# Optimization experiments

Hardware: AMD Instinct MI355X
Metric: run time of the kernel (lower is better)

The kernel has to match this reference:

```python
import jax, jax.numpy as jnp
import numpy as np
from jax.scipy.special import logsumexp

N, K, D = 131072, 256, 32


def setup_inputs() -> dict:
    key = jax.random.key(0)
    k1, k2, k3 = jax.random.split(key, 3)
    points = jax.random.normal(k1, (N, D), dtype=jnp.float32)
    centers = jax.random.uniform(k2, (K, D), dtype=jnp.float32)
    # well-conditioned inverse-sqrt covariances (original used 15*I; scaled to
    # avoid float32 overflow in sqrt(det(covs_inv)) for D=32)
    covs_inv_sqrt = (0.5 * jnp.broadcast_to(jnp.eye(D, dtype=jnp.float32), (K, D, D))
                     + 0.02 * jax.random.normal(k3, (K, D, D), dtype=jnp.float32))
    weights = jnp.ones((K,), dtype=jnp.float32)
    threshold = jnp.zeros((1,), dtype=jnp.float32)
    return {"points": points, "centers": centers,
            "covs_inv_sqrt": covs_inv_sqrt, "weights": weights,
            "threshold": threshold}


def reference(points, centers, covs_inv_sqrt, weights, threshold):
    # refresh(): equal_clusters=True branch
    w = jnp.abs(weights)
    center_prs = w / (w.sum() + 1e-30)                       # [K]
    covs_inv = jnp.einsum('kde,kfe->kdf', covs_inv_sqrt, covs_inv_sqrt)  # [K,D,D]
    coefs = center_prs * jnp.sqrt(jnp.linalg.det(covs_inv))  # [K]

    # pairwise weighted sqdist: q_ij = (x_i - c_j)^T A_j (x_i - c_j)
    B = covs_inv.reshape(K, D * D)                           # [K, D*D]
    X2 = (points[:, :, None] * points[:, None, :]).reshape(N, D * D)  # [N, D*D]
    t_xAx = X2 @ B.T                                         # [N, K]
    m = jnp.einsum('kde,ke->kd', covs_inv, centers)          # A_j c_j, [K,D]
    t_xAc = points @ m.T                                     # [N, K]
    t_cAc = jnp.einsum('kd,kd->k', m, centers)               # [K]
    d_ij = -0.5 * (t_xAx - 2.0 * t_xAc + t_cAc[None, :])     # [N, K]

    # weighted logsumexp over centers, then subtract threshold
    ll = logsumexp(d_ij, axis=1, b=coefs[None, :])           # [N]
    return ll[:, None] - threshold[0]                        # [N, 1]
```

## Files before the change

### kernel.cpp

```cpp
#include <hip/hip_runtime.h>
#include <math.h>

#define NPTS 131072
#define KCOMP 256
#define DIM 32
#define KF 608
#define PSIF_BYTES 311296
#define WS_NEED (PSIF_BYTES + KCOMP * 4)

typedef __attribute__((ext_vector_type(8))) short short8;
typedef __attribute__((ext_vector_type(16))) float f32x16;

__device__ __forceinline__ unsigned short f2bf(float v) {
    unsigned u = __float_as_uint(v);
    u += 0x7fffu + ((u >> 16) & 1u);
    return (unsigned short)(u >> 16);
}

__device__ __forceinline__ unsigned pkbf(float lo, float hi) {
#if __has_builtin(__builtin_amdgcn_perm)
    const unsigned a = __float_as_uint(hi) + 0x8000u;
    const unsigned b = __float_as_uint(lo) + 0x8000u;
    return __builtin_amdgcn_perm(a, b, 0x07060302u);
#else
    return (unsigned)f2bf(lo) | ((unsigned)f2bf(hi) << 16);
#endif
}

__device__ __forceinline__ void dma16(const uint4* g, uint4* s) {
    __builtin_amdgcn_global_load_lds(
        (const __attribute__((address_space(1))) void*)g,
        (__attribute__((address_space(3))) void*)s, 16, 0, 0);
}

__device__ __forceinline__ void barrier_lds_only() {
    asm volatile("s_waitcnt lgkmcnt(0)\ns_barrier" ::: "memory");
}

constexpr int L4c(int d) { return ((32 - d + 3) / 4) * 4; }
constexpr int PfxC(int d) { int s = 0; for (int i = 0; i < d; ++i) s += L4c(i); return s; }
constexpr int rowOfC(int p) { int d = 0; while (d < 31 && PfxC(d + 1) <= p) ++d; return d; }
constexpr int dOfC(int p) { return (p >= 576) ? -1 : rowOfC(p); }
constexpr int f0OfC(int p) {
    return (p >= 576) ? (p - 576) : ((rowOfC(p) & ~3) + (p - PfxC(rowOfC(p))));
}

__global__ __launch_bounds__(256) void gmm_pre(
    const float* __restrict__ S,
    const float* __restrict__ centers,
    const float* __restrict__ weights,
    unsigned short* __restrict__ PsiF,
    float* __restrict__ kc2)
{
    __shared__ float Sl[DIM][DIM + 1];
    __shared__ float As[DIM][DIM + 1];
    __shared__ float cl[DIM], ml[DIM];
    __shared__ float red[256];

    const int k = blockIdx.x, tid = threadIdx.x;

    for (int idx = tid; idx < DIM * DIM; idx += 256)
        Sl[idx >> 5][idx & 31] = S[(size_t)k * DIM * DIM + idx];
    if (tid < DIM) cl[tid] = centers[k * DIM + tid];
    __syncthreads();

    for (int idx = tid; idx < DIM * DIM; idx += 256) {
        const int d = idx >> 5, f = idx & 31;
        float a = 0.f;
#pragma unroll
        for (int e = 0; e < DIM; ++e) a = fmaf(Sl[d][e], Sl[f][e], a);
        As[d][f] = a;
    }
    __syncthreads();

    if (tid < DIM) {
        float mv = 0.f;
#pragma unroll
        for (int f = 0; f < DIM; ++f) mv = fmaf(As[tid][f], cl[f], mv);
        ml[tid] = mv;
    }
    __syncthreads();

    for (int p = tid; p < KF; p += 256) {
        float val;
        if (p < 576) {
            int d = 0, pr = 0;
            while (true) {
                const int len = ((32 - d + 3) >> 2) << 2;
                if (pr + len > p) break;
                pr += len; ++d;
            }
            const int f = (d & ~3) + (p - pr);
            val = (f < d) ? 0.f : ((f == d) ? -0.5f * As[d][d] : -As[d][f]);
        } else {
            val = ml[p - 576];
        }
        const int c = p >> 6, kk = p & 63;
        const int s = kk >> 4, qq = (kk >> 3) & 1, j = kk & 7;
        const int ct = k >> 5, ll = qq * 32 + (k & 31);
        const int g = c * 2048 + (s * 8 + ct) * 64 + ll;
        PsiF[(size_t)g * 8 + j] = f2bf(val);
    }

    red[tid] = fabsf(weights[tid]);
    __syncthreads();
    for (int off = 128; off > 0; off >>= 1) {
        if (tid < off) red[tid] += red[tid + off];
        __syncthreads();
    }
    const float wsum = red[0];

    for (int j = 0; j < DIM - 1; ++j) {
        const float inv = 1.0f / As[j][j];
        for (int idx = tid; idx < DIM * DIM; idx += 256) {
            const int r = idx >> 5, c = idx & 31;
            if (r > j && c > j)
                As[r][c] = fmaf(-As[r][j] * inv, As[j][c], As[r][c]);
        }
        __syncthreads();
    }

    if (tid < DIM) red[tid] = __logf(As[tid][tid]);
    __syncthreads();
    if (tid == 0) {
        float sl = 0.f;
        for (int j = 0; j < DIM; ++j) sl += red[j];
        float cac = 0.f;
        for (int d2 = 0; d2 < DIM; ++d2) cac = fmaf(ml[d2], cl[d2], cac);
        kc2[k] = __logf(fabsf(weights[k])) - __logf(wsum + 1e-30f)
               + 0.5f * sl - 0.5f * cac;
    }
}

template<int P>
__device__ __forceinline__ void genQuad(const float (&x)[DIM], float* v) {
    constexpr int d = dOfC(P);
    constexpr int f0 = f0OfC(P);
#pragma unroll
    for (int j = 0; j < 4; ++j)
        v[j] = (d < 0) ? x[f0 + j] : (x[d] * x[f0 + j]);
}

template<int C, int SS>
__device__ __forceinline__ void genSite(const float (&x)[DIM], uint4* sA4,
                                        int rbg, int r32) {
    float v[8];
    genQuad<C * 64 + SS * 8>(x, v);
    genQuad<C * 64 + SS * 8 + 4>(x, v + 4);
    uint4 u;
    u.x = pkbf(v[0], v[1]);
    u.y = pkbf(v[2], v[3]);
    u.z = pkbf(v[4], v[5]);
    u.w = pkbf(v[6], v[7]);
    sA4[(SS >> 1) * 256 + rbg * 64 + (SS & 1) * 32 + r32] = u;
}

template<int C>
__device__ __forceinline__ void doChunk(const float (&x)[DIM],
    uint4* sA4, uint4* sB4, const uint4* __restrict__ PsiF4,
    f32x16 (&acc0)[4], f32x16 (&acc1)[4],
    int l, int w, int q, int rbg, int r32, int r0, int c0)
{
    constexpr int NS  = (C < 9) ? 4 : 2;
    constexpr int NSn = (C < 8) ? 4 : ((C == 8) ? 2 : 0);

    if constexpr (C > 0) barrier_lds_only();
    if (q == 0) {
        genSite<C, 0>(x, sA4, rbg, r32);
        genSite<C, 2>(x, sA4, rbg, r32);
        if constexpr (NS == 4) { genSite<C, 4>(x, sA4, rbg, r32); genSite<C, 6>(x, sA4, rbg, r32); }
    } else {
        genSite<C, 1>(x, sA4, rbg, r32);
        genSite<C, 3>(x, sA4, rbg, r32);
        if constexpr (NS == 4) { genSite<C, 5>(x, sA4, rbg, r32); genSite<C, 7>(x, sA4, rbg, r32); }
    }
    __syncthreads();

    if constexpr (NSn > 0) {
        const uint4* src = PsiF4 + (C + 1) * 2048 + w * 64 + l;
        uint4* dst = sB4 + ((C + 1) & 1) * 2048 + w * 64 + l;
#pragma unroll
        for (int i = 0; i < NSn * 2; ++i) dma16(src + i * 256, dst + i * 256);
    }

    const uint4* bb = sB4 + (C & 1) * 2048;
#pragma unroll
    for (int s = 0; s < NS; ++s) {
        short8 a0 = __builtin_bit_cast(short8, sA4[(s * 4 + r0) * 64 + l]);
        short8 a1 = __builtin_bit_cast(short8, sA4[(s * 4 + r0 + 1) * 64 + l]);
#pragma unroll
        for (int j = 0; j < 4; ++j) {
            short8 b = __builtin_bit_cast(short8, bb[(s * 8 + c0 + j) * 64 + l]);
            acc0[j] = __builtin_amdgcn_mfma_f32_32x32x16_bf16(a0, b, acc0[j], 0, 0, 0);
            acc1[j] = __builtin_amdgcn_mfma_f32_32x32x16_bf16(a1, b, acc1[j], 0, 0, 0);
        }
    }
}

__device__ __forceinline__ void epiHalf(const f32x16 (&acc)[4], const float (&kcv)[4],
    int rblock, int l, int whalf, float (*sM)[2], float (*sS)[2])
{
#pragma unroll
    for (int rg = 0; rg < 16; ++rg) {
        float vals[4], m = -INFINITY;
#pragma unroll
        for (int j = 0; j < 4; ++j) { vals[j] = acc[j][rg] + kcv[j]; m = fmaxf(m, vals[j]); }
#pragma unroll
        for (int mask = 1; mask < 32; mask <<= 1) m = fmaxf(m, __shfl_xor(m, mask, 64));
        float sv = 0.f;
#pragma unroll
        for (int j = 0; j < 4; ++j) sv += __expf(vals[j] - m);
#pragma unroll
        for (int mask = 1; mask < 32; mask <<= 1) sv += __shfl_xor(sv, mask, 64);
        if ((l & 31) == 0) {
            const int R = rblock * 32 + (rg & 3) + 8 * (rg >> 2) + 4 * (l >> 5);
            sM[R][whalf] = m; sS[R][whalf] = sv;
        }
    }
}

__global__ __launch_bounds__(256, 2) void gmm_mfma(
    const float* __restrict__ points,
    const unsigned short* __restrict__ PsiF,
    const float* __restrict__ kc2,
    const float* __restrict__ thr,
    float* __restrict__ out)
{
    __shared__ uint4 sA4[1024];
    __shared__ uint4 sB4[4096];
    float (*sM)[2] = (float (*)[2])sA4;
    float (*sS)[2] = (float (*)[2])(sA4 + 64);

    const int t = threadIdx.x;
    const int w = t >> 6, l = t & 63;
    const int row = t & 127, q = t >> 7;
    const int rbg = row >> 5, r32 = row & 31;
    const int r0 = (w >> 1) * 2, c0 = (w & 1) * 4;

    const uint4* PsiF4 = (const uint4*)PsiF;

    {
        const uint4* src = PsiF4 + w * 64 + l;
        uint4* dst = sB4 + w * 64 + l;
#pragma unroll
        for (int i = 0; i < 8; ++i) dma16(src + i * 256, dst + i * 256);
    }

    float x[DIM];
    const float4* px = (const float4*)(points + ((size_t)blockIdx.x * 128 + row) * DIM);
#pragma unroll
    for (int j2 = 0; j2 < 8; ++j2) {
        float4 v = px[j2];
        x[4 * j2 + 0] = v.x; x[4 * j2 + 1] = v.y;
        x[4 * j2 + 2] = v.z; x[4 * j2 + 3] = v.w;
    }

    f32x16 acc0[4], acc1[4];
#pragma unroll
    for (int j = 0; j < 4; ++j)
#pragma unroll
        for (int r = 0; r < 16; ++r) { acc0[j][r] = 0.f; acc1[j][r] = 0.f; }

    doChunk<0>(x, sA4, sB4, PsiF4, acc0, acc1, l, w, q, rbg, r32, r0, c0);
    doChunk<1>(x, sA4, sB4, PsiF4, acc0, acc1, l, w, q, rbg, r32, r0, c0);
    doChunk<2>(x, sA4, sB4, PsiF4, acc0, acc1, l, w, q, rbg, r32, r0, c0);
    doChunk<3>(x, sA4, sB4, PsiF4, acc0, acc1, l, w, q, rbg, r32, r0, c0);
    doChunk<4>(x, sA4, sB4, PsiF4, acc0, acc1, l, w, q, rbg, r32, r0, c0);
    doChunk<5>(x, sA4, sB4, PsiF4, acc0, acc1, l, w, q, rbg, r32, r0, c0);
    doChunk<6>(x, sA4, sB4, PsiF4, acc0, acc1, l, w, q, rbg, r32, r0, c0);
    doChunk<7>(x, sA4, sB4, PsiF4, acc0, acc1, l, w, q, rbg, r32, r0, c0);
    doChunk<8>(x, sA4, sB4, PsiF4, acc0, acc1, l, w, q, rbg, r32, r0, c0);
    doChunk<9>(x, sA4, sB4, PsiF4, acc0, acc1, l, w, q, rbg, r32, r0, c0);

    float kcv[4];
#pragma unroll
    for (int j = 0; j < 4; ++j) kcv[j] = kc2[(c0 + j) * 32 + (l & 31)];

    __syncthreads();
    epiHalf(acc0, kcv, r0,     l, w & 1, sM, sS);
    epiHalf(acc1, kcv, r0 + 1, l, w & 1, sM, sS);
    __syncthreads();

    if (t < 128) {
        const float m0 = sM[t][0], m1 = sM[t][1];
        const float M = fmaxf(m0, m1);
        const float Sv = sS[t][0] * __expf(m0 - M) + sS[t][1] * __expf(m1 - M);
        out[(size_t)blockIdx.x * 128 + t] = M + __logf(Sv) - thr[0];
    }
}

extern "C" void kernel_launch(void* const* d_in, const int* in_sizes, int n_in,
                              void* d_out, int out_size, void* d_ws, size_t ws_size,
                              hipStream_t stream) {
    const float* points  = (const float*)d_in[0];
    const float* centers = (const float*)d_in[1];
    const float* covs    = (const float*)d_in[2];
    const float* weights = (const float*)d_in[3];
    const float* thr     = (const float*)d_in[4];
    float* out = (float*)d_out;

    unsigned short* PsiF = (unsigned short*)d_ws;
    float* kc2 = (float*)((char*)d_ws + PSIF_BYTES);

    gmm_pre<<<KCOMP, 256, 0, stream>>>(covs, centers, weights, PsiF, kc2);
    gmm_mfma<<<NPTS / 128, 256, 0, stream>>>(points, PsiF, kc2, thr, out);
}
```

Measured before the change: 150.4 us.

## Double block to 512 threads, pack points as fp16, shrink per-wave accumulators

Moves the main MFMA kernel from 256 to 512 threads per block, with 8 waves each owning a 2x2 tile of 32x32 accumulators instead of 2x4. Each thread now builds one quarter of the A-operand sites, and the logsumexp partials are merged across four column groups. Each thread keeps its point in registers as packed fp16 to cut register pressure and allow higher occupancy. The cost is an extra fp16 rounding of the inputs before the bf16 quadratic products, plus a wider cross-wave reduction.

```diff
diff --git a/kernel.cpp b/kernel.cpp
--- a/kernel.cpp
+++ b/kernel.cpp
@@ -1,4 +1,5 @@
 #include <hip/hip_runtime.h>
+#include <hip/hip_fp16.h>
 #include <math.h>
 
 #define NPTS 131072
@@ -132,21 +133,35 @@
     }
 }
 
+template<int IDX>
+__device__ __forceinline__ float upk(const unsigned (&xp)[16]) {
+    unsigned h = xp[IDX >> 1];
+    if constexpr (IDX & 1) h >>= 16; else h &= 0xffffu;
+    return __half2float(__builtin_bit_cast(__half, (unsigned short)h));
+}
+
 template<int P>
-__device__ __forceinline__ void genQuad(const float (&x)[DIM], float* v) {
+__device__ __forceinline__ void genQuad(const unsigned (&xp)[16], float* v) {
     constexpr int d = dOfC(P);
     constexpr int f0 = f0OfC(P);
-#pragma unroll
-    for (int j = 0; j < 4; ++j)
-        v[j] = (d < 0) ? x[f0 + j] : (x[d] * x[f0 + j]);
+    float xd = 1.f;
+    if constexpr (d >= 0) xd = upk<d>(xp);
+    const float a0 = upk<f0 + 0>(xp);
+    const float a1 = upk<f0 + 1>(xp);
+    const float a2 = upk<f0 + 2>(xp);
+    const float a3 = upk<f0 + 3>(xp);
+    v[0] = (d < 0) ? a0 : xd * a0;
+    v[1] = (d < 0) ? a1 : xd * a1;
+    v[2] = (d < 0) ? a2 : xd * a2;
+    v[3] = (d < 0) ? a3 : xd * a3;
 }
 
 template<int C, int SS>
-__device__ __forceinline__ void genSite(const float (&x)[DIM], uint4* sA4,
+__device__ __forceinline__ void genSite(const unsigned (&xp)[16], uint4* sA4,
                                         int rbg, int r32) {
     float v[8];
-    genQuad<C * 64 + SS * 8>(x, v);
-    genQuad<C * 64 + SS * 8 + 4>(x, v + 4);
+    genQuad<C * 64 + SS * 8>(xp, v);
+    genQuad<C * 64 + SS * 8 + 4>(xp, v + 4);
     uint4 u;
     u.x = pkbf(v[0], v[1]);
     u.y = pkbf(v[2], v[3]);
@@ -156,70 +171,49 @@
 }
 
 template<int C>
-__device__ __forceinline__ void doChunk(const float (&x)[DIM],
+__device__ __forceinline__ void doChunk(const unsigned (&xp)[16],
     uint4* sA4, uint4* sB4, const uint4* __restrict__ PsiF4,
-    f32x16 (&acc0)[4], f32x16 (&acc1)[4],
-    int l, int w, int q, int rbg, int r32, int r0, int c0)
+    f32x16 (&acc)[2][2],
+    int t, int l, int q2, int rbg, int r32, int rh, int cq)
 {
     constexpr int NS  = (C < 9) ? 4 : 2;
     constexpr int NSn = (C < 8) ? 4 : ((C == 8) ? 2 : 0);
 
     if constexpr (C > 0) barrier_lds_only();
-    if (q == 0) {
-        genSite<C, 0>(x, sA4, rbg, r32);
-        genSite<C, 2>(x, sA4, rbg, r32);
-        if constexpr (NS == 4) { genSite<C, 4>(x, sA4, rbg, r32); genSite<C, 6>(x, sA4, rbg, r32); }
-    } else {
-        genSite<C, 1>(x, sA4, rbg, r32);
-        genSite<C, 3>(x, sA4, rbg, r32);
-        if constexpr (NS == 4) { genSite<C, 5>(x, sA4, rbg, r32); genSite<C, 7>(x, sA4, rbg, r32); }
+    switch (q2) {
+    case 0: genSite<C, 0>(xp, sA4, rbg, r32);
+            if constexpr (NS == 4) genSite<C, 4>(xp, sA4, rbg, r32); break;
+    case 1: genSite<C, 1>(xp, sA4, rbg, r32);
+            if constexpr (NS == 4) genSite<C, 5>(xp, sA4, rbg, r32); break;
+    case 2: genSite<C, 2>(xp, sA4, rbg, r32);
+            if constexpr (NS == 4) genSite<C, 6>(xp, sA4, rbg, r32); break;
+    default: genSite<C, 3>(xp, sA4, rbg, r32);
+            if constexpr (NS == 4) genSite<C, 7>(xp, sA4, rbg, r32); break;
     }
     __syncthreads();
 
     if constexpr (NSn > 0) {
-        const uint4* src = PsiF4 + (C + 1) * 2048 + w * 64 + l;
-        uint4* dst = sB4 + ((C + 1) & 1) * 2048 + w * 64 + l;
-#pragma unroll
-        for (int i = 0; i < NSn * 2; ++i) dma16(src + i * 256, dst + i * 256);
+        const uint4* src = PsiF4 + (C + 1) * 2048 + t;
+        uint4* dst = sB4 + ((C + 1) & 1) * 2048 + t;
+#pragma unroll
+        for (int i = 0; i < NSn; ++i) dma16(src + i * 512, dst + i * 512);
     }
 
     const uint4* bb = sB4 + (C & 1) * 2048;
 #pragma unroll
     for (int s = 0; s < NS; ++s) {
-        short8 a0 = __builtin_bit_cast(short8, sA4[(s * 4 + r0) * 64 + l]);
-        short8 a1 = __builtin_bit_cast(short8, sA4[(s * 4 + r0 + 1) * 64 + l]);
-#pragma unroll
-        for (int j = 0; j < 4; ++j) {
-            short8 b = __builtin_bit_cast(short8, bb[(s * 8 + c0 + j) * 64 + l]);
-            acc0[j] = __builtin_amdgcn_mfma_f32_32x32x16_bf16(a0, b, acc0[j], 0, 0, 0);
-            acc1[j] = __builtin_amdgcn_mfma_f32_32x32x16_bf16(a1, b, acc1[j], 0, 0, 0);
-        }
-    }
-}
-
-__device__ __forceinline__ void epiHalf(const f32x16 (&acc)[4], const float (&kcv)[4],
-    int rblock, int l, int whalf, float (*sM)[2], float (*sS)[2])
-{
-#pragma unroll
-    for (int rg = 0; rg < 16; ++rg) {
-        float vals[4], m = -INFINITY;
-#pragma unroll
-        for (int j = 0; j < 4; ++j) { vals[j] = acc[j][rg] + kcv[j]; m = fmaxf(m, vals[j]); }
-#pragma unroll
-        for (int mask = 1; mask < 32; mask <<= 1) m = fmaxf(m, __shfl_xor(m, mask, 64));
-        float sv = 0.f;
-#pragma unroll
-        for (int j = 0; j < 4; ++j) sv += __expf(vals[j] - m);
-#pragma unroll
-        for (int mask = 1; mask < 32; mask <<= 1) sv += __shfl_xor(sv, mask, 64);
-        if ((l & 31) == 0) {
-            const int R = rblock * 32 + (rg & 3) + 8 * (rg >> 2) + 4 * (l >> 5);
-            sM[R][whalf] = m; sS[R][whalf] = sv;
-        }
-    }
-}
-
-__global__ __launch_bounds__(256, 2) void gmm_mfma(
+        short8 a0 = __builtin_bit_cast(short8, sA4[(s * 4 + rh * 2 + 0) * 64 + l]);
+        short8 a1 = __builtin_bit_cast(short8, sA4[(s * 4 + rh * 2 + 1) * 64 + l]);
+        short8 b0 = __builtin_bit_cast(short8, bb[(s * 8 + cq * 2 + 0) * 64 + l]);
+        short8 b1 = __builtin_bit_cast(short8, bb[(s * 8 + cq * 2 + 1) * 64 + l]);
+        acc[0][0] = __builtin_amdgcn_mfma_f32_32x32x16_bf16(a0, b0, acc[0][0], 0, 0, 0);
+        acc[0][1] = __builtin_amdgcn_mfma_f32_32x32x16_bf16(a0, b1, acc[0][1], 0, 0, 0);
+        acc[1][0] = __builtin_amdgcn_mfma_f32_32x32x16_bf16(a1, b0, acc[1][0], 0, 0, 0);
+        acc[1][1] = __builtin_amdgcn_mfma_f32_32x32x16_bf16(a1, b1, acc[1][1], 0, 0, 0);
+    }
+}
+
+__global__ __launch_bounds__(512, 4) void gmm_mfma(
     const float* __restrict__ points,
     const unsigned short* __restrict__ PsiF,
     const float* __restrict__ kc2,
@@ -228,63 +222,88 @@
 {
     __shared__ uint4 sA4[1024];
     __shared__ uint4 sB4[4096];
-    float (*sM)[2] = (float (*)[2])sA4;
-    float (*sS)[2] = (float (*)[2])(sA4 + 64);
+    float (*sPm)[4] = (float (*)[4])sA4;
+    float (*sPs)[4] = (float (*)[4])(sA4 + 128);
 
     const int t = threadIdx.x;
     const int w = t >> 6, l = t & 63;
-    const int row = t & 127, q = t >> 7;
+    const int row = t & 127, q2 = t >> 7;
     const int rbg = row >> 5, r32 = row & 31;
-    const int r0 = (w >> 1) * 2, c0 = (w & 1) * 4;
+    const int rh = w >> 2, cq = w & 3;
 
     const uint4* PsiF4 = (const uint4*)PsiF;
 
     {
-        const uint4* src = PsiF4 + w * 64 + l;
-        uint4* dst = sB4 + w * 64 + l;
-#pragma unroll
-        for (int i = 0; i < 8; ++i) dma16(src + i * 256, dst + i * 256);
-    }
-
-    float x[DIM];
-    const float4* px = (const float4*)(points + ((size_t)blockIdx.x * 128 + row) * DIM);
-#pragma unroll
-    for (int j2 = 0; j2 < 8; ++j2) {
-        float4 v = px[j2];
-        x[4 * j2 + 0] = v.x; x[4 * j2 + 1] = v.y;
-        x[4 * j2 + 2] = v.z; x[4 * j2 + 3] = v.w;
-    }
-
-    f32x16 acc0[4], acc1[4];
-#pragma unroll
-    for (int j = 0; j < 4; ++j)
-#pragma unroll
-        for (int r = 0; r < 16; ++r) { acc0[j][r] = 0.f; acc1[j][r] = 0.f; }
-
-    doChunk<0>(x, sA4, sB4, PsiF4, acc0, acc1, l, w, q, rbg, r32, r0, c0);
-    doChunk<1>(x, sA4, sB4, PsiF4, acc0, acc1, l, w, q, rbg, r32, r0, c0);
-    doChunk<2>(x, sA4, sB4, PsiF4, acc0, acc1, l, w, q, rbg, r32, r0, c0);
-    doChunk<3>(x, sA4, sB4, PsiF4, acc0, acc1, l, w, q, rbg, r32, r0, c0);
-    doChunk<4>(x, sA4, sB4, PsiF4, acc0, acc1, l, w, q, rbg, r32, r0, c0);
-    doChunk<5>(x, sA4, sB4, PsiF4, acc0, acc1, l, w, q, rbg, r32, r0, c0);
-    doChunk<6>(x, sA4, sB4, PsiF4, acc0, acc1, l, w, q, rbg, r32, r0, c0);
-    doChunk<7>(x, sA4, sB4, PsiF4, acc0, acc1, l, w, q, rbg, r32, r0, c0);
-    doChunk<8>(x, sA4, sB4, PsiF4, acc0, acc1, l, w, q, rbg, r32, r0, c0);
-    doChunk<9>(x, sA4, sB4, PsiF4, acc0, acc1, l, w, q, rbg, r32, r0, c0);
-
-    float kcv[4];
-#pragma unroll
-    for (int j = 0; j < 4; ++j) kcv[j] = kc2[(c0 + j) * 32 + (l & 31)];
-
-    __syncthreads();
-    epiHalf(acc0, kcv, r0,     l, w & 1, sM, sS);
-    epiHalf(acc1, kcv, r0 + 1, l, w & 1, sM, sS);
+        const uint4* src = PsiF4 + t;
+        uint4* dst = sB4 + t;
+#pragma unroll
+        for (int i = 0; i < 4; ++i) dma16(src + i * 512, dst + i * 512);
+    }
+
+    unsigned xp[16];
+    {
+        const float4* px = (const float4*)(points + ((size_t)blockIdx.x * 128 + row) * DIM);
+#pragma unroll
+        for (int j2 = 0; j2 < 8; ++j2) {
+            float4 v = px[j2];
+            xp[2 * j2 + 0] = __builtin_bit_cast(unsigned, __floats2half2_rn(v.x, v.y));
+            xp[2 * j2 + 1] = __builtin_bit_cast(unsigned, __floats2half2_rn(v.z, v.w));
+        }
+    }
+
+    f32x16 acc[2][2];
+#pragma unroll
+    for (int a = 0; a < 2; ++a)
+#pragma unroll
+        for (int b = 0; b < 2; ++b)
+#pragma unroll
+            for (int r = 0; r < 16; ++r) acc[a][b][r] = 0.f;
+
+    doChunk<0>(xp, sA4, sB4, PsiF4, acc, t, l, q2, rbg, r32, rh, cq);
+    doChunk<1>(xp, sA4, sB4, PsiF4, acc, t, l, q2, rbg, r32, rh, cq);
+    doChunk<2>(xp, sA4, sB4, PsiF4, acc, t, l, q2, rbg, r32, rh, cq);
+    doChunk<3>(xp, sA4, sB4, PsiF4, acc, t, l, q2, rbg, r32, rh, cq);
+    doChunk<4>(xp, sA4, sB4, PsiF4, acc, t, l, q2, rbg, r32, rh, cq);
+    doChunk<5>(xp, sA4, sB4, PsiF4, acc, t, l, q2, rbg, r32, rh, cq);
+    doChunk<6>(xp, sA4, sB4, PsiF4, acc, t, l, q2, rbg, r32, rh, cq);
+    doChunk<7>(xp, sA4, sB4, PsiF4, acc, t, l, q2, rbg, r32, rh, cq);
+    doChunk<8>(xp, sA4, sB4, PsiF4, acc, t, l, q2, rbg, r32, rh, cq);
+    doChunk<9>(xp, sA4, sB4, PsiF4, acc, t, l, q2, rbg, r32, rh, cq);
+
+    float kcv[2];
+#pragma unroll
+    for (int j = 0; j < 2; ++j) kcv[j] = kc2[(cq * 2 + j) * 32 + (l & 31)];
+
+    __syncthreads();
+
+#pragma unroll
+    for (int rb = 0; rb < 2; ++rb) {
+#pragma unroll
+        for (int rg = 0; rg < 16; ++rg) {
+            const float v0 = acc[rb][0][rg] + kcv[0];
+            const float v1 = acc[rb][1][rg] + kcv[1];
+            float m = fmaxf(v0, v1);
+#pragma unroll
+            for (int mask = 1; mask < 32; mask <<= 1)
+                m = fmaxf(m, __shfl_xor(m, mask, 64));
+            float sv = __expf(v0 - m) + __expf(v1 - m);
+#pragma unroll
+            for (int mask = 1; mask < 32; mask <<= 1)
+                sv += __shfl_xor(sv, mask, 64);
+            if ((l & 31) == 0) {
+                const int R = rh * 64 + rb * 32 + (rg & 3) + 8 * (rg >> 2) + 4 * (l >> 5);
+                sPm[R][cq] = m; sPs[R][cq] = sv;
+            }
+        }
+    }
     __syncthreads();
 
     if (t < 128) {
-        const float m0 = sM[t][0], m1 = sM[t][1];
-        const float M = fmaxf(m0, m1);
-        const float Sv = sS[t][0] * __expf(m0 - M) + sS[t][1] * __expf(m1 - M);
+        const float m0 = sPm[t][0], m1 = sPm[t][1];
+        const float m2 = sPm[t][2], m3 = sPm[t][3];
+        const float M = fmaxf(fmaxf(m0, m1), fmaxf(m2, m3));
+        const float Sv = sPs[t][0] * __expf(m0 - M) + sPs[t][1] * __expf(m1 - M)
+                       + sPs[t][2] * __expf(m2 - M) + sPs[t][3] * __expf(m3 - M);
         out[(size_t)blockIdx.x * 128 + t] = M + __logf(Sv) - thr[0];
     }
 }
@@ -303,5 +322,5 @@
     float* kc2 = (float*)((char*)d_ws + PSIF_BYTES);
 
     gmm_pre<<<KCOMP, 256, 0, stream>>>(covs, centers, weights, PsiF, kc2);
-    gmm_mfma<<<NPTS / 128, 256, 0, stream>>>(points, PsiF, kc2, thr, out);
-}
+    gmm_mfma<<<NPTS / 128, 512, 0, stream>>>(points, PsiF, kc2, thr, out);
+}
```

After: 154.6 us. 2.8% more time.
